# Kernel optimization log

Measured on AMD Instinct MI355X. Metric: run time of the kernel, lower is better.

Reference implementation:

```python
import jax, jax.numpy as jnp
import numpy as np

B, N, H, T = 64, 64, 128, 128


def setup_inputs() -> dict:
    key = jax.random.key(0)
    ks = jax.random.split(key, 8)
    tf = jax.random.normal(ks[0], (B, N, H, T), dtype=jnp.float32)
    # learnable symmetric adjacency parameter
    ap = jax.random.normal(ks[1], (N, N), dtype=jnp.float32) * 0.1
    ap = (ap + ap.T) / 2
    # edge MLP params (stored as (in, out) for x @ W)
    W1 = jax.random.normal(ks[2], (2 * H, H), dtype=jnp.float32) * (1.0 / np.sqrt(2 * H))
    b1 = jnp.zeros((H,), dtype=jnp.float32)
    W2 = jax.random.normal(ks[3], (H, H // 2), dtype=jnp.float32) * (1.0 / np.sqrt(H))
    b2 = jnp.zeros((H // 2,), dtype=jnp.float32)
    W3 = jax.random.normal(ks[4], (H // 2, 1), dtype=jnp.float32) * (1.0 / np.sqrt(H // 2))
    b3 = jnp.zeros((1,), dtype=jnp.float32)
    return {"temporal_features": tf, "adj_param": ap, "W1": W1, "b1": b1,
            "W2": W2, "b2": b2, "W3": W3, "b3": b3}


def reference(temporal_features, adj_param, W1, b1, W2, b2, W3, b3):
    # node features: mean over time -> (B, N, H)
    node = temporal_features.mean(axis=-1)
    h_dim = node.shape[-1]
    # concat([h_i, h_j]) @ W1 == h_i @ W1[:H] + h_j @ W1[H:]  (avoids materializing 2H concat)
    Wi, Wj = W1[:h_dim], W1[h_dim:]
    pi = jnp.einsum('bnh,hk->bnk', node, Wi)  # (B, N, H)
    pj = jnp.einsum('bnh,hk->bnk', node, Wj)
    h = jax.nn.relu(pi[:, :, None, :] + pj[:, None, :, :] + b1)  # (B, N, N, H)
    # Dropout(0.2) is identity at inference
    h = jax.nn.relu(jnp.einsum('bijh,hk->bijk', h, W2) + b2)      # (B, N, N, H//2)
    feat_adj = (jnp.einsum('bijk,ko->bijo', h, W3) + b3)[..., 0]  # (B, N, N)
    # combined method
    adj = 0.5 * adj_param[None, :, :] + 0.5 * feat_adj
    # symmetrize + relu
    adj = jax.nn.relu((adj + jnp.swapaxes(adj, -2, -1)) / 2)
    # add self-loops and degree-normalize rows
    adj = adj + jnp.eye(adj.shape[-1], dtype=adj.dtype)[None]
    adj = adj / (adj.sum(axis=-1, keepdims=True) + 1e-8)
    return adj
```

## Files before the change

### kernel.cpp

```cpp
#include <hip/hip_runtime.h>
#include <stdint.h>
#include <stddef.h>

typedef __attribute__((ext_vector_type(8))) short short8;
typedef __attribute__((ext_vector_type(4))) float f32x4;
typedef __attribute__((ext_vector_type(4))) unsigned uint4v;

__device__ inline unsigned short f2bf(float x) {
    unsigned u = __float_as_uint(x);
    unsigned r = (u + 0x7fffu + ((u >> 16) & 1u)) >> 16;
    return (unsigned short)r;
}

__device__ inline unsigned pkasm(float a, float b) {
    unsigned r;
    asm("v_cvt_pk_bf16_f32 %0, %1, %2" : "=v"(r) : "v"(a), "v"(b));
    return r;
}

__global__ __launch_bounds__(256) void k1_mean(const float* __restrict__ tf,
                                               float* __restrict__ node) {
    int wave = (blockIdx.x * blockDim.x + threadIdx.x) >> 6;
    int lane = threadIdx.x & 63;
    int half = lane >> 5;
    int c = lane & 31;
    const f32x4* tf4 = reinterpret_cast<const f32x4*>(tf);
    size_t base = (size_t)wave * 8 * 64;

    f32x4 v[8];
#pragma unroll
    for (int k = 0; k < 8; ++k) v[k] = __builtin_nontemporal_load(&tf4[base + (size_t)k * 64 + lane]);

    float s[8];
#pragma unroll
    for (int k = 0; k < 8; ++k) s[k] = (v[k][0] + v[k][1]) + (v[k][2] + v[k][3]);
#pragma unroll
    for (int m = 1; m <= 16; m <<= 1) {
#pragma unroll
        for (int k = 0; k < 8; ++k) s[k] += __shfl_xor(s[k], m);
    }
    if (c == 0) {
#pragma unroll
        for (int k = 0; k < 8; ++k) {
            int rp = wave * 8 + k;
            node[(size_t)rp * 2 + half] = s[k] * (1.0f / 128.0f);
        }
    }
}

__global__ __launch_bounds__(256) void k2_proj(const float* __restrict__ node,
                                               const float* __restrict__ W1,
                                               const float* __restrict__ b1,
                                               float* __restrict__ pi,
                                               float* __restrict__ pj) {
    const int LP = 136;
    __shared__ unsigned short A_lds[32 * LP];
    __shared__ unsigned short BT[128 * LP];
    __shared__ float b1s[128];

    int tid = threadIdx.x;
    int rblk = blockIdx.x >> 1;
    int half = blockIdx.x & 1;
    int r0 = rblk * 32;

    {
        int row = tid >> 3;
        int c0 = (tid & 7) * 16;
        const float4* src = reinterpret_cast<const float4*>(node + (size_t)(r0 + row) * 128 + c0);
        short8 pk[2];
#pragma unroll
        for (int q = 0; q < 2; ++q) {
            float4 va = src[q * 2 + 0];
            float4 vb = src[q * 2 + 1];
            pk[q][0] = (short)f2bf(va.x); pk[q][1] = (short)f2bf(va.y);
            pk[q][2] = (short)f2bf(va.z); pk[q][3] = (short)f2bf(va.w);
            pk[q][4] = (short)f2bf(vb.x); pk[q][5] = (short)f2bf(vb.y);
            pk[q][6] = (short)f2bf(vb.z); pk[q][7] = (short)f2bf(vb.w);
        }
        short8* dst = reinterpret_cast<short8*>(&A_lds[row * LP + c0]);
        dst[0] = pk[0];
        dst[1] = pk[1];
    }
    {
        int n = tid & 127;
        int kh = tid >> 7;
        const float* Wbase = W1 + (size_t)half * 128 * 128 + n;
#pragma unroll
        for (int g = 0; g < 8; ++g) {
            int kb = kh * 64 + g * 8;
            short8 pk;
#pragma unroll
            for (int e = 0; e < 8; ++e) pk[e] = (short)f2bf(Wbase[(size_t)(kb + e) * 128]);
            *reinterpret_cast<short8*>(&BT[n * LP + kb]) = pk;
        }
    }
    if (tid < 128) b1s[tid] = b1[tid];
    __syncthreads();

    int w = tid >> 6;
    int l = tid & 63;
    int lr = l & 15;
    int lg = l >> 4;
    int rt = w & 1;
    int ch = w >> 1;

    f32x4 acc[4] = {{0,0,0,0},{0,0,0,0},{0,0,0,0},{0,0,0,0}};
#pragma unroll
    for (int ks = 0; ks < 4; ++ks) {
        int kb = ks * 32 + lg * 8;
        short8 afrag = *reinterpret_cast<const short8*>(&A_lds[(rt * 16 + lr) * LP + kb]);
#pragma unroll
        for (int nt = 0; nt < 4; ++nt) {
            short8 bfrag = *reinterpret_cast<const short8*>(&BT[(ch * 64 + nt * 16 + lr) * LP + kb]);
            acc[nt] = __builtin_amdgcn_mfma_f32_16x16x32_bf16(afrag, bfrag, acc[nt], 0, 0, 0);
        }
    }
    float* out = half ? pj : pi;
#pragma unroll
    for (int nt = 0; nt < 4; ++nt) {
        int col = ch * 64 + nt * 16 + lr;
        float bias = half ? 0.0f : b1s[col];
#pragma unroll
        for (int r = 0; r < 4; ++r) {
            int row = r0 + rt * 16 + lg * 4 + r;
            out[(size_t)row * 128 + col] = acc[nt][r] + bias;
        }
    }
}

__global__ __launch_bounds__(256, 4) void k3_mlp(const float* __restrict__ pi,
                                                 const float* __restrict__ pj,
                                                 const float* __restrict__ W2,
                                                 const float* __restrict__ b2,
                                                 const float* __restrict__ W3,
                                                 const float* __restrict__ b3,
                                                 float* __restrict__ F) {
    const int LDA = 136;
    __shared__ unsigned short A_lds[64 * LDA];
    __shared__ unsigned short W2T[64 * LDA];
    __shared__ float pipb4[4][128];
    __shared__ float b2s[64], w3s[64];

    int tid = threadIdx.x;
    int b = blockIdx.x >> 4;
    int it = blockIdx.x & 15;
    int i0 = it * 4;
    int jt = tid >> 2;
    int kq = tid & 3;

    float pjreg[32];
    {
        const float* src = pj + ((size_t)(b * 64 + jt) * 128 + kq * 32);
#pragma unroll
        for (int e = 0; e < 8; ++e) {
            float4 v = reinterpret_cast<const float4*>(src)[e];
            pjreg[e * 4 + 0] = v.x;
            pjreg[e * 4 + 1] = v.y;
            pjreg[e * 4 + 2] = v.z;
            pjreg[e * 4 + 3] = v.w;
        }
    }
    if (tid < 128) {
        int row = tid >> 5;
        int c4 = tid & 31;
        float4 v = reinterpret_cast<const float4*>(pi + ((size_t)(b * 64 + i0 + row) * 128))[c4];
        reinterpret_cast<float4*>(&pipb4[row][0])[c4] = v;
    }
    {
        int m = jt;
#pragma unroll
        for (int g = 0; g < 4; ++g) {
            unsigned wb[4];
#pragma unroll
            for (int p = 0; p < 4; ++p) {
                int k = kq * 32 + g * 8 + p * 2;
                wb[p] = pkasm(W2[(size_t)k * 64 + m], W2[(size_t)(k + 1) * 64 + m]);
            }
            *reinterpret_cast<uint4v*>(&W2T[m * LDA + kq * 32 + g * 8]) = *reinterpret_cast<uint4v*>(wb);
        }
    }
    if (tid < 64) {
        b2s[tid] = b2[tid];
        w3s[tid] = W3[tid];
    }
    float b3v = b3[0];
    __syncthreads();

    int w = tid >> 6;
    int l = tid & 63;
    int lr = l & 15;
    int lg = l >> 4;

    short8 bfr0[4], bfr1[4];
#pragma unroll
    for (int ks = 0; ks < 4; ++ks) {
        int kb = ks * 32 + lg * 8;
        bfr0[ks] = *reinterpret_cast<const short8*>(&W2T[(0 * 16 + lr) * LDA + kb]);
        bfr1[ks] = *reinterpret_cast<const short8*>(&W2T[(1 * 16 + lr) * LDA + kb]);
    }

    for (int il = 0; il < 4; ++il) {
        {
            unsigned* dst = reinterpret_cast<unsigned*>(&A_lds[jt * LDA + kq * 32]);
#pragma unroll
            for (int e2 = 0; e2 < 16; ++e2) {
                float a0 = fmaxf(pipb4[il][kq * 32 + e2 * 2 + 0] + pjreg[e2 * 2 + 0], 0.0f);
                float a1 = fmaxf(pipb4[il][kq * 32 + e2 * 2 + 1] + pjreg[e2 * 2 + 1], 0.0f);
                dst[e2] = pkasm(a0, a1);
            }
        }
        __syncthreads();
        f32x4 acc0 = {0.f, 0.f, 0.f, 0.f};
        f32x4 acc1 = {0.f, 0.f, 0.f, 0.f};
        f32x4 acc2 = {0.f, 0.f, 0.f, 0.f};
        f32x4 acc3 = {0.f, 0.f, 0.f, 0.f};
#pragma unroll
        for (int ks = 0; ks < 4; ++ks) {
            int kb = ks * 32 + lg * 8;
            short8 afrag = *reinterpret_cast<const short8*>(&A_lds[(w * 16 + lr) * LDA + kb]);
            short8 b2f = *reinterpret_cast<const short8*>(&W2T[(2 * 16 + lr) * LDA + kb]);
            short8 b3f = *reinterpret_cast<const short8*>(&W2T[(3 * 16 + lr) * LDA + kb]);
            acc0 = __builtin_amdgcn_mfma_f32_16x16x32_bf16(afrag, bfr0[ks], acc0, 0, 0, 0);
            acc1 = __builtin_amdgcn_mfma_f32_16x16x32_bf16(afrag, bfr1[ks], acc1, 0, 0, 0);
            acc2 = __builtin_amdgcn_mfma_f32_16x16x32_bf16(afrag, b2f, acc2, 0, 0, 0);
            acc3 = __builtin_amdgcn_mfma_f32_16x16x32_bf16(afrag, b3f, acc3, 0, 0, 0);
        }
        float part[4] = {0.f, 0.f, 0.f, 0.f};
#pragma unroll
        for (int mt = 0; mt < 4; ++mt) {
            int m = mt * 16 + lr;
            float w3 = w3s[m];
            float bb = b2s[m];
            f32x4 a = (mt == 0) ? acc0 : (mt == 1) ? acc1 : (mt == 2) ? acc2 : acc3;
#pragma unroll
            for (int r = 0; r < 4; ++r) {
                float h = fmaxf(a[r] + bb, 0.0f);
                part[r] += h * w3;
            }
        }
#pragma unroll
        for (int r = 0; r < 4; ++r) {
            part[r] += __shfl_xor(part[r], 1);
            part[r] += __shfl_xor(part[r], 2);
            part[r] += __shfl_xor(part[r], 4);
            part[r] += __shfl_xor(part[r], 8);
        }
        if (lr == 0) {
#pragma unroll
            for (int r = 0; r < 4; ++r) {
                int j = w * 16 + lg * 4 + r;
                F[((size_t)b * 64 + i0 + il) * 64 + j] = part[r] + b3v;
            }
        }
        __syncthreads();
    }
}

__global__ __launch_bounds__(256) void k4_final(const float* __restrict__ F,
                                                const float* __restrict__ ap,
                                                float* __restrict__ out) {
    __shared__ float s[64][65];
    int b = blockIdx.x;
    int tid = threadIdx.x;
    for (int idx = tid; idx < 4096; idx += 256) {
        s[idx >> 6][idx & 63] = F[(size_t)b * 4096 + idx];
    }
    __syncthreads();
    int w = tid >> 6, lane = tid & 63;
#pragma unroll
    for (int itr = 0; itr < 16; ++itr) {
        int i = w + 4 * itr;
        float a_ij = ap[i * 64 + lane];
        float v = 0.5f * a_ij + 0.25f * (s[i][lane] + s[lane][i]);
        v = fmaxf(v, 0.0f);
        if (i == lane) v += 1.0f;
        float sum = v;
        sum += __shfl_xor(sum, 1);
        sum += __shfl_xor(sum, 2);
        sum += __shfl_xor(sum, 4);
        sum += __shfl_xor(sum, 8);
        sum += __shfl_xor(sum, 16);
        sum += __shfl_xor(sum, 32);
        out[(size_t)b * 4096 + i * 64 + lane] = v / (sum + 1e-8f);
    }
}

extern "C" void kernel_launch(void* const* d_in, const int* in_sizes, int n_in,
                              void* d_out, int out_size, void* d_ws, size_t ws_size,
                              hipStream_t stream) {
    const float* tf = (const float*)d_in[0];
    const float* ap = (const float*)d_in[1];
    const float* W1 = (const float*)d_in[2];
    const float* b1 = (const float*)d_in[3];
    const float* W2 = (const float*)d_in[4];
    const float* b2 = (const float*)d_in[5];
    const float* W3 = (const float*)d_in[6];
    const float* b3 = (const float*)d_in[7];
    float* out = (float*)d_out;

    char* ws = (char*)d_ws;
    float* node = (float*)(ws);
    float* pi   = (float*)(ws + (size_t)(2 << 20));
    float* pj   = (float*)(ws + (size_t)(4 << 20));
    float* F    = (float*)(ws + (size_t)(6 << 20));

    k1_mean<<<8192, 256, 0, stream>>>(tf, node);
    k2_proj<<<256, 256, 0, stream>>>(node, W1, b1, pi, pj);
    k3_mlp<<<1024, 256, 0, stream>>>(pi, pj, W2, b2, W3, b3, F);
    k4_final<<<64, 256, 0, stream>>>(F, ap, out);
}
```

Before: 81.16 us.

## Build MLP A-fragments directly in registers, removing A LDS staging and barriers

The first-layer activations (relu(pi+pj)) are now computed straight into the MFMA A-fragment registers, with each lane loading the pj row matching its fragment layout. The A_lds buffer and the two per-iteration __syncthreads are removed, which cuts LDS traffic and synchronisation. In exchange, the bf16 conversion now uses a software rounding routine instead of the packed v_cvt_pk_bf16_f32 instruction, adding VALU work per element. The occupancy hint on launch_bounds is also dropped.

```diff
diff --git a/kernel.cpp b/kernel.cpp
--- a/kernel.cpp
+++ b/kernel.cpp
@@ -10,12 +10,6 @@
     unsigned u = __float_as_uint(x);
     unsigned r = (u + 0x7fffu + ((u >> 16) & 1u)) >> 16;
     return (unsigned short)r;
-}
-
-__device__ inline unsigned pkasm(float a, float b) {
-    unsigned r;
-    asm("v_cvt_pk_bf16_f32 %0, %1, %2" : "=v"(r) : "v"(a), "v"(b));
-    return r;
 }
 
 __global__ __launch_bounds__(256) void k1_mean(const float* __restrict__ tf,
@@ -128,15 +122,14 @@
     }
 }
 
-__global__ __launch_bounds__(256, 4) void k3_mlp(const float* __restrict__ pi,
-                                                 const float* __restrict__ pj,
-                                                 const float* __restrict__ W2,
-                                                 const float* __restrict__ b2,
-                                                 const float* __restrict__ W3,
-                                                 const float* __restrict__ b3,
-                                                 float* __restrict__ F) {
+__global__ __launch_bounds__(256) void k3_mlp(const float* __restrict__ pi,
+                                              const float* __restrict__ pj,
+                                              const float* __restrict__ W2,
+                                              const float* __restrict__ b2,
+                                              const float* __restrict__ W3,
+                                              const float* __restrict__ b3,
+                                              float* __restrict__ F) {
     const int LDA = 136;
-    __shared__ unsigned short A_lds[64 * LDA];
     __shared__ unsigned short W2T[64 * LDA];
     __shared__ float pipb4[4][128];
     __shared__ float b2s[64], w3s[64];
@@ -148,16 +141,22 @@
     int jt = tid >> 2;
     int kq = tid & 3;
 
+    int w = tid >> 6;
+    int l = tid & 63;
+    int lr = l & 15;
+    int lg = l >> 4;
+
     float pjreg[32];
     {
-        const float* src = pj + ((size_t)(b * 64 + jt) * 128 + kq * 32);
-#pragma unroll
-        for (int e = 0; e < 8; ++e) {
-            float4 v = reinterpret_cast<const float4*>(src)[e];
-            pjreg[e * 4 + 0] = v.x;
-            pjreg[e * 4 + 1] = v.y;
-            pjreg[e * 4 + 2] = v.z;
-            pjreg[e * 4 + 3] = v.w;
+        const float* pjrow = pj + (size_t)(b * 64 + w * 16 + lr) * 128;
+#pragma unroll
+        for (int ks = 0; ks < 4; ++ks) {
+            float4 q0 = *reinterpret_cast<const float4*>(pjrow + ks * 32 + lg * 8);
+            float4 q1 = *reinterpret_cast<const float4*>(pjrow + ks * 32 + lg * 8 + 4);
+            pjreg[ks * 8 + 0] = q0.x; pjreg[ks * 8 + 1] = q0.y;
+            pjreg[ks * 8 + 2] = q0.z; pjreg[ks * 8 + 3] = q0.w;
+            pjreg[ks * 8 + 4] = q1.x; pjreg[ks * 8 + 5] = q1.y;
+            pjreg[ks * 8 + 6] = q1.z; pjreg[ks * 8 + 7] = q1.w;
         }
     }
     if (tid < 128) {
@@ -174,7 +173,8 @@
 #pragma unroll
             for (int p = 0; p < 4; ++p) {
                 int k = kq * 32 + g * 8 + p * 2;
-                wb[p] = pkasm(W2[(size_t)k * 64 + m], W2[(size_t)(k + 1) * 64 + m]);
+                wb[p] = (unsigned)f2bf(W2[(size_t)k * 64 + m]) |
+                        ((unsigned)f2bf(W2[(size_t)(k + 1) * 64 + m]) << 16);
             }
             *reinterpret_cast<uint4v*>(&W2T[m * LDA + kq * 32 + g * 8]) = *reinterpret_cast<uint4v*>(wb);
         }
@@ -185,11 +185,6 @@
     }
     float b3v = b3[0];
     __syncthreads();
-
-    int w = tid >> 6;
-    int l = tid & 63;
-    int lr = l & 15;
-    int lg = l >> 4;
 
     short8 bfr0[4], bfr1[4];
 #pragma unroll
@@ -200,24 +195,25 @@
     }
 
     for (int il = 0; il < 4; ++il) {
-        {
-            unsigned* dst = reinterpret_cast<unsigned*>(&A_lds[jt * LDA + kq * 32]);
-#pragma unroll
-            for (int e2 = 0; e2 < 16; ++e2) {
-                float a0 = fmaxf(pipb4[il][kq * 32 + e2 * 2 + 0] + pjreg[e2 * 2 + 0], 0.0f);
-                float a1 = fmaxf(pipb4[il][kq * 32 + e2 * 2 + 1] + pjreg[e2 * 2 + 1], 0.0f);
-                dst[e2] = pkasm(a0, a1);
-            }
-        }
-        __syncthreads();
         f32x4 acc0 = {0.f, 0.f, 0.f, 0.f};
         f32x4 acc1 = {0.f, 0.f, 0.f, 0.f};
         f32x4 acc2 = {0.f, 0.f, 0.f, 0.f};
         f32x4 acc3 = {0.f, 0.f, 0.f, 0.f};
+        const float4* prow = reinterpret_cast<const float4*>(&pipb4[il][0]);
 #pragma unroll
         for (int ks = 0; ks < 4; ++ks) {
             int kb = ks * 32 + lg * 8;
-            short8 afrag = *reinterpret_cast<const short8*>(&A_lds[(w * 16 + lr) * LDA + kb]);
+            float4 pa = prow[ks * 8 + lg * 2];
+            float4 pb = prow[ks * 8 + lg * 2 + 1];
+            short8 afrag;
+            afrag[0] = (short)f2bf(fmaxf(pa.x + pjreg[ks * 8 + 0], 0.0f));
+            afrag[1] = (short)f2bf(fmaxf(pa.y + pjreg[ks * 8 + 1], 0.0f));
+            afrag[2] = (short)f2bf(fmaxf(pa.z + pjreg[ks * 8 + 2], 0.0f));
+            afrag[3] = (short)f2bf(fmaxf(pa.w + pjreg[ks * 8 + 3], 0.0f));
+            afrag[4] = (short)f2bf(fmaxf(pb.x + pjreg[ks * 8 + 4], 0.0f));
+            afrag[5] = (short)f2bf(fmaxf(pb.y + pjreg[ks * 8 + 5], 0.0f));
+            afrag[6] = (short)f2bf(fmaxf(pb.z + pjreg[ks * 8 + 6], 0.0f));
+            afrag[7] = (short)f2bf(fmaxf(pb.w + pjreg[ks * 8 + 7], 0.0f));
             short8 b2f = *reinterpret_cast<const short8*>(&W2T[(2 * 16 + lr) * LDA + kb]);
             short8 b3f = *reinterpret_cast<const short8*>(&W2T[(3 * 16 + lr) * LDA + kb]);
             acc0 = __builtin_amdgcn_mfma_f32_16x16x32_bf16(afrag, bfr0[ks], acc0, 0, 0, 0);
@@ -252,7 +248,6 @@
                 F[((size_t)b * 64 + i0 + il) * 64 + j] = part[r] + b3v;
             }
         }
-        __syncthreads();
     }
 }
 
```

Measured after the change: 73.88 us. 9.0% less time.
